# Kernel tuning notes

Hardware: AMD Instinct MI355X
Metric: run time of the kernel (lower is better)

## Reference

```python
import jax, jax.numpy as jnp
import numpy as np

B, L, S, H, E, D = 8, 1024, 1024, 8, 64, 64


def setup_inputs() -> dict:
    key = jax.random.key(0)
    kq, kk, kv, ka = jax.random.split(key, 4)
    queries = jax.random.normal(kq, (B, L, H, E), dtype=jnp.float32)
    keys = jax.random.normal(kk, (B, S, H, E), dtype=jnp.float32)
    values = jax.random.normal(kv, (B, S, H, D), dtype=jnp.float32)
    # previous layer's attention logits (residual bias), scaled down a bit
    A = jax.random.normal(ka, (B, H, L, S), dtype=jnp.float32) * 0.1
    # causal mask: True = masked (strict upper triangle), shape (B,1,L,S)
    attn_mask = jnp.broadcast_to(
        jnp.triu(jnp.ones((L, S), dtype=bool), k=1)[None, None], (B, 1, L, S)
    )
    return {"queries": queries, "keys": keys, "values": values,
            "attn_mask": attn_mask, "A": A}


def reference(queries, keys, values, attn_mask, A):
    # queries: (B,L,H,E), keys/values: (B,S,H,E/D), A: (B,H,L,S)
    E_ = queries.shape[-1]
    scale = 1.0 / jnp.sqrt(jnp.asarray(E_, dtype=queries.dtype))
    scores = jnp.einsum('blhe,bshe->bhls', queries, keys)  # (B,H,L,S)
    neg_inf = jnp.asarray(-jnp.inf, dtype=scores.dtype)
    scores = jnp.where(attn_mask, neg_inf, scores)
    # layer_nums > 0: residual bias from previous layer's logits
    A_new = jax.nn.softmax(scale * scores + A, axis=-1)
    # dropout p=0.0 -> identity (eval-mode reference)
    V = jnp.einsum('bhls,bshd->blhd', A_new, values)  # (B,L,H,D)
    return V, A_new
```

## Files before the change

### kernel.cpp

```cpp
#include <hip/hip_runtime.h>

#define B_ 8
#define L_ 1024
#define S_ 1024
#define H_ 8
#define E_ 64
#define D_ 64

typedef __attribute__((ext_vector_type(8))) short bf16x8;
typedef __attribute__((ext_vector_type(4))) float f32x4;
typedef __attribute__((ext_vector_type(4))) ushort u16x4;

__device__ __forceinline__ ushort f2b(float f) {
    unsigned u = __float_as_uint(f);
    return (ushort)((u + 0x7fffu + ((u >> 16) & 1u)) >> 16);
}
__device__ __forceinline__ float b2f(ushort b) {
    return __uint_as_float(((unsigned)b) << 16);
}

__device__ __forceinline__ int pswz(int r, int c) {
    return (((r << 11) + (c << 1)) ^ ((r & 7) << 4)) >> 1;
}

__device__ __forceinline__ bf16x8 load8_f2b(const float* p) {
    float4 a = *(const float4*)(p);
    float4 b = *(const float4*)(p + 4);
    bf16x8 r;
    r[0] = (short)f2b(a.x); r[1] = (short)f2b(a.y);
    r[2] = (short)f2b(a.z); r[3] = (short)f2b(a.w);
    r[4] = (short)f2b(b.x); r[5] = (short)f2b(b.y);
    r[6] = (short)f2b(b.z); r[7] = (short)f2b(b.w);
    return r;
}

__global__ __launch_bounds__(256) void vt_kernel(const float* __restrict__ V,
                                                 ushort* __restrict__ VT) {
    __shared__ ushort tile[64][72];
    int bh = blockIdx.x >> 4;
    int st = blockIdx.x & 15;
    int t  = threadIdx.x;
    int b = bh >> 3, h = bh & 7;

    int s_loc = t >> 2;
    int dg = (t & 3) << 4;
    const float* src = V + (((size_t)(b * S_ + st * 64 + s_loc) * H_ + h) * D_ + dg);
#pragma unroll
    for (int v = 0; v < 4; ++v) {
        float4 f = *(const float4*)(src + v * 4);
        tile[s_loc][dg + v * 4 + 0] = f2b(f.x);
        tile[s_loc][dg + v * 4 + 1] = f2b(f.y);
        tile[s_loc][dg + v * 4 + 2] = f2b(f.z);
        tile[s_loc][dg + v * 4 + 3] = f2b(f.w);
    }
    __syncthreads();

    int d = t >> 2;
    int sg = (t & 3) << 4;
    ushort tmp[16];
#pragma unroll
    for (int i = 0; i < 16; ++i) tmp[i] = tile[sg + i][d];
    ushort* dst = VT + (((size_t)bh * D_ + d) * S_ + st * 64 + sg);
    *(uint4*)(dst)     = *(uint4*)&tmp[0];
    *(uint4*)(dst + 8) = *(uint4*)&tmp[8];
}

__global__ __launch_bounds__(256) void kb_kernel(const float* __restrict__ K,
                                                 ushort* __restrict__ KB) {
    size_t i = ((size_t)blockIdx.x * 256 + threadIdx.x) * 8;
    float4 a = *(const float4*)(K + i);
    float4 b = *(const float4*)(K + i + 4);
    ushort o[8];
    o[0] = f2b(a.x); o[1] = f2b(a.y); o[2] = f2b(a.z); o[3] = f2b(a.w);
    o[4] = f2b(b.x); o[5] = f2b(b.y); o[6] = f2b(b.z); o[7] = f2b(b.w);
    *(uint4*)(KB + i) = *(uint4*)o;
}

template <int USE_WS>
__global__ __launch_bounds__(256, 4) void attn_kernel(
    const float* __restrict__ Q, const float* __restrict__ K,
    const float* __restrict__ A, const ushort* __restrict__ KB,
    const ushort* __restrict__ VT, const float* __restrict__ V,
    float* __restrict__ outV, float* __restrict__ outA) {
    __shared__ __align__(16) ushort pb[16 * S_];
    __shared__ float red[4][16];

    int idx  = blockIdx.x;
    int lt   = 63 - (idx & 63);
    int bh   = idx >> 6;
    int b    = bh >> 3, h = bh & 7;
    int l0   = lt << 4;
    int t    = threadIdx.x;
    int wave = t >> 6, lane = t & 63;
    int quad = lane >> 4, lm = lane & 15;

    const size_t qbase = ((size_t)(b * L_ + l0 + lm) * H_ + h) * E_ + quad * 8;
    bf16x8 qf0 = load8_f2b(Q + qbase);
    bf16x8 qf1 = load8_f2b(Q + qbase + 32);

    const float scale = 0.125f;
    int nsb  = lt + 1;
    int nsbe = (nsb + 1) & ~1;
    const float* Ab = A + ((size_t)bh * L_ + l0) * S_;
    int rg = l0 + lm;

    float psum = 0.f;
    for (int sb = wave; sb < nsbe; sb += 4) {
        int s0 = sb << 4;
        f32x4 acc = {0.f, 0.f, 0.f, 0.f};
        float4 a4 = {0.f, 0.f, 0.f, 0.f};
        int c0 = s0 + quad * 4;
        if (sb < nsb) {
            const size_t kbase = ((size_t)(b * S_ + s0 + lm) * H_ + h) * E_ + quad * 8;
            bf16x8 kf0, kf1;
            if (USE_WS) {
                kf0 = *(const bf16x8*)(KB + kbase);
                kf1 = *(const bf16x8*)(KB + kbase + 32);
            } else {
                kf0 = load8_f2b(K + kbase);
                kf1 = load8_f2b(K + kbase + 32);
            }
            a4 = *(const float4*)(Ab + (size_t)lm * S_ + c0);
            acc = __builtin_amdgcn_mfma_f32_16x16x32_bf16(kf0, qf0, acc, 0, 0, 0);
            acc = __builtin_amdgcn_mfma_f32_16x16x32_bf16(kf1, qf1, acc, 0, 0, 0);
        }
        u16x4 ps;
#pragma unroll
        for (int r = 0; r < 4; ++r) {
            float av = (r == 0) ? a4.x : (r == 1) ? a4.y : (r == 2) ? a4.z : a4.w;
            float z = acc[r] * scale + av;
            float p = (c0 + r <= rg) ? __expf(z) : 0.f;
            psum += p;
            ps[r] = f2b(p);
        }
        *(u16x4*)&pb[pswz(lm, c0)] = ps;
    }

    psum += __shfl_xor(psum, 16);
    psum += __shfl_xor(psum, 32);
    if (quad == 0) red[wave][lm] = psum;
    __syncthreads();

#pragma unroll
    for (int i = 0; i < 4; ++i) {
        int R  = wave * 4 + i;
        int rgl = l0 + R;
        float inv = 1.0f / (red[0][R] + red[1][R] + red[2][R] + red[3][R]);
        float* Orow = outA + ((size_t)bh * L_ + rgl) * S_;
#pragma unroll
        for (int hf = 0; hf < 2; ++hf) {
            int c = hf * 512 + lane * 8;
            bf16x8 pv = *(const bf16x8*)&pb[pswz(R, c)];
            float o[8];
#pragma unroll
            for (int j = 0; j < 8; ++j)
                o[j] = (c + j <= rgl) ? b2f((ushort)pv[j]) * inv : 0.f;
            *(float4*)(Orow + c)     = *(float4*)&o[0];
            *(float4*)(Orow + c + 4) = *(float4*)&o[4];
        }
    }

    int nks = (lt >> 1) + 1;
    int d0  = wave << 4;
    f32x4 oacc = {0.f, 0.f, 0.f, 0.f};
    for (int ks = 0; ks < nks; ++ks) {
        int sbb = ks << 5;
        bf16x8 pf = *(const bf16x8*)&pb[pswz(lm, sbb + quad * 8)];
        bf16x8 vf;
        if (USE_WS) {
            vf = *(const bf16x8*)(VT + ((size_t)(bh * D_ + d0 + lm) * S_ + sbb + quad * 8));
        } else {
#pragma unroll
            for (int j = 0; j < 8; ++j)
                vf[j] = (short)f2b(V[((size_t)(b * S_ + sbb + quad * 8 + j) * H_ + h) * D_ + d0 + lm]);
        }
        oacc = __builtin_amdgcn_mfma_f32_16x16x32_bf16(pf, vf, oacc, 0, 0, 0);
    }
#pragma unroll
    for (int r = 0; r < 4; ++r) {
        int R = quad * 4 + r;
        float inv = 1.0f / (red[0][R] + red[1][R] + red[2][R] + red[3][R]);
        int l = l0 + R;
        outV[((size_t)(b * L_ + l) * H_ + h) * D_ + d0 + lm] = oacc[r] * inv;
    }
}

extern "C" void kernel_launch(void* const* d_in, const int* in_sizes, int n_in,
                              void* d_out, int out_size, void* d_ws, size_t ws_size,
                              hipStream_t stream) {
    const float* Q = (const float*)d_in[0];
    const float* K = (const float*)d_in[1];
    const float* V = (const float*)d_in[2];
    const float* A = (const float*)d_in[4];
    float* outV = (float*)d_out;
    float* outA = outV + (size_t)B_ * L_ * H_ * D_;

    size_t vt_elems = (size_t)B_ * H_ * D_ * S_;
    size_t kb_elems = (size_t)B_ * S_ * H_ * E_;
    size_t need = (vt_elems + kb_elems) * sizeof(ushort);
    ushort* VT = (ushort*)d_ws;
    ushort* KB = VT + vt_elems;

    if (ws_size >= need) {
        vt_kernel<<<B_ * H_ * (S_ / 64), 256, 0, stream>>>(V, VT);
        kb_kernel<<<(int)(kb_elems / (256 * 8)), 256, 0, stream>>>(K, KB);
        attn_kernel<1><<<B_ * H_ * (L_ / 16), 256, 0, stream>>>(Q, K, A, KB, VT, V, outV, outA);
    } else {
        attn_kernel<0><<<B_ * H_ * (L_ / 16), 256, 0, stream>>>(Q, K, A, KB, VT, V, outV, outA);
    }
}
```

Baseline: 582.0 us.

## Fuse PV matmul into score loop with register-stashed probabilities

Removes the 32KB shared-memory probability buffer. Probabilities are kept in registers (a 16-entry stash) and multiplied with V immediately using 16x16x16 MFMAs, with each wave accumulating partial outputs that are reduced through a small shared buffer. The A output is written straight from registers, and the occupancy hint is raised to 5 blocks per CU. The aim is to cut LDS use and the separate PV pass so more blocks can be resident. The cost is higher register pressure, more, smaller MFMAs and narrower VT loads.

```diff
diff --git a/kernel.cpp b/kernel.cpp
--- a/kernel.cpp
+++ b/kernel.cpp
@@ -8,6 +8,7 @@
 #define D_ 64
 
 typedef __attribute__((ext_vector_type(8))) short bf16x8;
+typedef __attribute__((ext_vector_type(4))) short bf16x4;
 typedef __attribute__((ext_vector_type(4))) float f32x4;
 typedef __attribute__((ext_vector_type(4))) ushort u16x4;
 
@@ -19,9 +20,21 @@
     return __uint_as_float(((unsigned)b) << 16);
 }
 
-__device__ __forceinline__ int pswz(int r, int c) {
-    return (((r << 11) + (c << 1)) ^ ((r & 7) << 4)) >> 1;
-}
+#if __has_builtin(__builtin_amdgcn_mfma_f32_16x16x16bf16_1k)
+__device__ __forceinline__ f32x4 mfma16(bf16x4 a, bf16x4 b, f32x4 c) {
+    return __builtin_amdgcn_mfma_f32_16x16x16bf16_1k(a, b, c, 0, 0, 0);
+}
+#elif __has_builtin(__builtin_amdgcn_mfma_f32_16x16x16_bf16)
+__device__ __forceinline__ f32x4 mfma16(bf16x4 a, bf16x4 b, f32x4 c) {
+    return __builtin_amdgcn_mfma_f32_16x16x16_bf16(a, b, c, 0, 0, 0);
+}
+#else
+__device__ __forceinline__ f32x4 mfma16(bf16x4 a, bf16x4 b, f32x4 c) {
+    f32x4 d;
+    asm("v_mfma_f32_16x16x16_bf16 %0, %1, %2, %3" : "=v"(d) : "v"(a), "v"(b), "v"(c));
+    return d;
+}
+#endif
 
 __device__ __forceinline__ bf16x8 load8_f2b(const float* p) {
     float4 a = *(const float4*)(p);
@@ -77,13 +90,13 @@
 }
 
 template <int USE_WS>
-__global__ __launch_bounds__(256, 4) void attn_kernel(
+__global__ __launch_bounds__(256, 5) void attn_kernel(
     const float* __restrict__ Q, const float* __restrict__ K,
     const float* __restrict__ A, const ushort* __restrict__ KB,
     const ushort* __restrict__ VT, const float* __restrict__ V,
     float* __restrict__ outV, float* __restrict__ outA) {
-    __shared__ __align__(16) ushort pb[16 * S_];
     __shared__ float red[4][16];
+    __shared__ float obuf[4][16][66];
 
     int idx  = blockIdx.x;
     int lt   = 63 - (idx & 63);
@@ -99,18 +112,20 @@
     bf16x8 qf1 = load8_f2b(Q + qbase + 32);
 
     const float scale = 0.125f;
-    int nsb  = lt + 1;
-    int nsbe = (nsb + 1) & ~1;
-    const float* Ab = A + ((size_t)bh * L_ + l0) * S_;
-    int rg = l0 + lm;
+    int nsb = lt + 1;
+    int rg  = l0 + lm;
+    const float* Arow = A + ((size_t)bh * L_ + l0 + lm) * S_ + quad * 4;
+    const ushort* VTrow = VT + ((size_t)bh * D_ + lm) * S_;
 
     float psum = 0.f;
-    for (int sb = wave; sb < nsbe; sb += 4) {
-        int s0 = sb << 4;
-        f32x4 acc = {0.f, 0.f, 0.f, 0.f};
-        float4 a4 = {0.f, 0.f, 0.f, 0.f};
-        int c0 = s0 + quad * 4;
+    u16x4 stash[16];
+    f32x4 oacc[4] = {{0.f,0.f,0.f,0.f},{0.f,0.f,0.f,0.f},{0.f,0.f,0.f,0.f},{0.f,0.f,0.f,0.f}};
+#pragma unroll
+    for (int i = 0; i < 16; ++i) {
+        int sb = wave + i * 4;
         if (sb < nsb) {
+            int s0 = sb << 4;
+            int c0 = s0 + quad * 4;
             const size_t kbase = ((size_t)(b * S_ + s0 + lm) * H_ + h) * E_ + quad * 8;
             bf16x8 kf0, kf1;
             if (USE_WS) {
@@ -120,68 +135,75 @@
                 kf0 = load8_f2b(K + kbase);
                 kf1 = load8_f2b(K + kbase + 32);
             }
-            a4 = *(const float4*)(Ab + (size_t)lm * S_ + c0);
+            float4 a4 = *(const float4*)(Arow + s0);
+            f32x4 acc = {0.f, 0.f, 0.f, 0.f};
             acc = __builtin_amdgcn_mfma_f32_16x16x32_bf16(kf0, qf0, acc, 0, 0, 0);
             acc = __builtin_amdgcn_mfma_f32_16x16x32_bf16(kf1, qf1, acc, 0, 0, 0);
+            u16x4 ps;
+            bf16x4 pf;
+#pragma unroll
+            for (int r = 0; r < 4; ++r) {
+                float av = (r == 0) ? a4.x : (r == 1) ? a4.y : (r == 2) ? a4.z : a4.w;
+                float z = acc[r] * scale + av;
+                float p = (c0 + r <= rg) ? __expf(z) : 0.f;
+                psum += p;
+                ps[r] = f2b(p);
+                pf[r] = (short)ps[r];
+            }
+            stash[i] = ps;
+#pragma unroll
+            for (int dd = 0; dd < 4; ++dd) {
+                bf16x4 vf;
+                if (USE_WS) {
+                    u16x4 vr = *(const u16x4*)(VTrow + (size_t)dd * 16 * S_ + c0);
+                    vf[0] = (short)vr[0]; vf[1] = (short)vr[1];
+                    vf[2] = (short)vr[2]; vf[3] = (short)vr[3];
+                } else {
+#pragma unroll
+                    for (int j = 0; j < 4; ++j)
+                        vf[j] = (short)f2b(V[((size_t)(b * S_ + c0 + j) * H_ + h) * D_ + dd * 16 + lm]);
+                }
+                oacc[dd] = mfma16(pf, vf, oacc[dd]);
+            }
         }
-        u16x4 ps;
-#pragma unroll
-        for (int r = 0; r < 4; ++r) {
-            float av = (r == 0) ? a4.x : (r == 1) ? a4.y : (r == 2) ? a4.z : a4.w;
-            float z = acc[r] * scale + av;
-            float p = (c0 + r <= rg) ? __expf(z) : 0.f;
-            psum += p;
-            ps[r] = f2b(p);
-        }
-        *(u16x4*)&pb[pswz(lm, c0)] = ps;
     }
 
     psum += __shfl_xor(psum, 16);
     psum += __shfl_xor(psum, 32);
     if (quad == 0) red[wave][lm] = psum;
+#pragma unroll
+    for (int dd = 0; dd < 4; ++dd)
+#pragma unroll
+        for (int r = 0; r < 4; ++r)
+            obuf[wave][quad * 4 + r][dd * 16 + lm] = oacc[dd][r];
     __syncthreads();
 
+    float invA = 1.0f / (red[0][lm] + red[1][lm] + red[2][lm] + red[3][lm]);
+    float* Aout = outA + ((size_t)bh * L_ + l0 + lm) * S_ + quad * 4;
+#pragma unroll
+    for (int i = 0; i < 16; ++i) {
+        int sb = wave + i * 4;
+        int s0 = sb << 4;
+        float4 o;
+        if (sb < nsb) {
+            u16x4 ps = stash[i];
+            o.x = b2f(ps[0]) * invA;
+            o.y = b2f(ps[1]) * invA;
+            o.z = b2f(ps[2]) * invA;
+            o.w = b2f(ps[3]) * invA;
+        } else {
+            o = make_float4(0.f, 0.f, 0.f, 0.f);
+        }
+        *(float4*)(Aout + s0) = o;
+    }
+
 #pragma unroll
     for (int i = 0; i < 4; ++i) {
-        int R  = wave * 4 + i;
-        int rgl = l0 + R;
-        float inv = 1.0f / (red[0][R] + red[1][R] + red[2][R] + red[3][R]);
-        float* Orow = outA + ((size_t)bh * L_ + rgl) * S_;
-#pragma unroll
-        for (int hf = 0; hf < 2; ++hf) {
-            int c = hf * 512 + lane * 8;
-            bf16x8 pv = *(const bf16x8*)&pb[pswz(R, c)];
-            float o[8];
-#pragma unroll
-            for (int j = 0; j < 8; ++j)
-                o[j] = (c + j <= rgl) ? b2f((ushort)pv[j]) * inv : 0.f;
-            *(float4*)(Orow + c)     = *(float4*)&o[0];
-            *(float4*)(Orow + c + 4) = *(float4*)&o[4];
-        }
-    }
-
-    int nks = (lt >> 1) + 1;
-    int d0  = wave << 4;
-    f32x4 oacc = {0.f, 0.f, 0.f, 0.f};
-    for (int ks = 0; ks < nks; ++ks) {
-        int sbb = ks << 5;
-        bf16x8 pf = *(const bf16x8*)&pb[pswz(lm, sbb + quad * 8)];
-        bf16x8 vf;
-        if (USE_WS) {
-            vf = *(const bf16x8*)(VT + ((size_t)(bh * D_ + d0 + lm) * S_ + sbb + quad * 8));
-        } else {
-#pragma unroll
-            for (int j = 0; j < 8; ++j)
-                vf[j] = (short)f2b(V[((size_t)(b * S_ + sbb + quad * 8 + j) * H_ + h) * D_ + d0 + lm]);
-        }
-        oacc = __builtin_amdgcn_mfma_f32_16x16x32_bf16(pf, vf, oacc, 0, 0, 0);
-    }
-#pragma unroll
-    for (int r = 0; r < 4; ++r) {
-        int R = quad * 4 + r;
-        float inv = 1.0f / (red[0][R] + red[1][R] + red[2][R] + red[3][R]);
-        int l = l0 + R;
-        outV[((size_t)(b * L_ + l) * H_ + h) * D_ + d0 + lm] = oacc[r] * inv;
+        int slot = t + i * 256;
+        int l = slot >> 6, d = slot & 63;
+        float sum = obuf[0][l][d] + obuf[1][l][d] + obuf[2][l][d] + obuf[3][l][d];
+        float inv = 1.0f / (red[0][l] + red[1][l] + red[2][l] + red[3][l]);
+        outV[((size_t)(b * L_ + l0 + l) * H_ + h) * D_ + d] = sum * inv;
     }
 }
 
```

Result: slower. 661.3 us (+13.6%).
